# Optimization experiments

Measured on AMD Instinct MI355X. Metric: run time of the kernel, lower is better.

The kernel has to match this reference:

```python
import jax, jax.numpy as jnp
import numpy as np

B, CH, T, D = 16, 64, 2048, 1  # d must be 1 (tf.squeeze(x, axis=-1))
F = 8  # conv filters


def setup_inputs() -> dict:
    key = jax.random.key(0)
    k1, k2, k3, k4 = jax.random.split(key, 4)
    return {
        "x": jax.random.normal(k1, (B, CH, T, D), dtype=jnp.float32),
        "w1": jax.random.normal(k2, (D, F), dtype=jnp.float32) * 0.1,
        "b1": jnp.zeros((F,), dtype=jnp.float32),
        "w2": jax.random.normal(k3, (D, F), dtype=jnp.float32) * 0.1,
        "b2": jnp.zeros((F,), dtype=jnp.float32),
        "gamma": jax.random.normal(k4, (1,), dtype=jnp.float32) * 0.1,
    }


def reference(x, w1, b1, w2, b2, gamma):
    b, ch, t, d = x.shape
    # 1x1 Conv2D == per-position matmul over channel dim; then Permute((2,1,3)) + Reshape((t,-1))
    q = (jnp.matmul(x, w1) + b1)  # (b, ch, t, F)
    k = (jnp.matmul(x, w2) + b2)  # (b, ch, t, F)
    q = jnp.transpose(q, (0, 2, 1, 3)).reshape(b, t, ch * q.shape[-1])  # (b, t, ch*F)
    k = jnp.transpose(k, (0, 2, 1, 3)).reshape(b, t, ch * k.shape[-1])  # (b, t, ch*F)
    energy = jnp.einsum('btf,bsf->bts', q, k)  # (b, t, t)
    max_h = jnp.max(energy, axis=2, keepdims=True)
    min_h = jnp.min(energy, axis=2, keepdims=True)
    energy = (energy - min_h) / (max_h - min_h + 1e-8)
    attention = jax.nn.softmax(energy, axis=-1)  # (b, t, t)
    x_sq = x[..., 0]  # (b, ch, t)
    # matmul(x_sq, attention, transpose_b=True): out[b,c,i] = sum_j x_sq[b,c,j] * attention[b,i,j]
    mixed = jnp.einsum('bcj,bij->bci', x_sq, attention)  # (b, ch, t)
    return gamma[0] * mixed[..., None] + x  # (b, ch, t, 1)
```

## Files before the change

kernel.cpp:

```cpp
#include <hip/hip_runtime.h>

#define NB 16
#define NCH 64
#define NT 2048
#define TI 32
#define TJ 64
#define STR 72

typedef __attribute__((ext_vector_type(8))) short bf8;
typedef __attribute__((ext_vector_type(4))) short bf4;
typedef __attribute__((ext_vector_type(4))) float f4;

static __device__ __forceinline__ short f2b(float f) {
    unsigned u = __float_as_uint(f);
    u += 0x7fffu + ((u >> 16) & 1u);
    return (short)(u >> 16);
}

__global__ __launch_bounds__(256)
void prep_k(const float* __restrict__ x, float* __restrict__ Xs,
            short* __restrict__ xT, short* __restrict__ xn) {
    __shared__ float T[NCH][65];
    const int b = blockIdx.y, t0 = blockIdx.x * 64;
    const int tid = threadIdx.x;
    const float* xb = x + (size_t)b * NCH * NT;

    const int tt = (tid & 15) * 4;
    #pragma unroll
    for (int co = 0; co < 4; ++co) {
        int c = co * 16 + (tid >> 4);
        float4 v = *reinterpret_cast<const float4*>(&xb[(size_t)c * NT + t0 + tt]);
        T[c][tt] = v.x; T[c][tt + 1] = v.y; T[c][tt + 2] = v.z; T[c][tt + 3] = v.w;
        bf4 w; w[0] = f2b(v.x); w[1] = f2b(v.y); w[2] = f2b(v.z); w[3] = f2b(v.w);
        *reinterpret_cast<bf4*>(&xn[((size_t)b * NCH + c) * NT + t0 + tt]) = w;
    }
    __syncthreads();
    if (tid < 64) {
        float s = 0.f;
        #pragma unroll
        for (int c = 0; c < NCH; ++c) s += T[c][tid];
        Xs[b * NT + t0 + tid] = s;
    }
    const int row = tid >> 2, cs = (tid & 3) * 16;
    bf8 v0, v1;
    #pragma unroll
    for (int u = 0; u < 8; ++u) v0[u] = f2b(T[cs + u][row]);
    #pragma unroll
    for (int u = 0; u < 8; ++u) v1[u] = f2b(T[cs + 8 + u][row]);
    short* dst = xT + ((size_t)b * NT + t0 + row) * NCH + cs;
    *reinterpret_cast<bf8*>(dst) = v0;
    *reinterpret_cast<bf8*>(dst + 8) = v1;
}

__global__ __launch_bounds__(256)
void attn3_k(const float* __restrict__ x,
             const float* __restrict__ w1, const float* __restrict__ b1p,
             const float* __restrict__ w2, const float* __restrict__ b2p,
             const float* __restrict__ gp,
             const float* __restrict__ Xs, const short* __restrict__ xT,
             const short* __restrict__ xn,
             float* __restrict__ out) {
    __shared__ short xiT[TI][STR];
    __shared__ short xjT[TJ][STR];
    __shared__ short xjn[NCH][STR];
    __shared__ short P[TI][STR];
    __shared__ float XjL[TJ];
    __shared__ float redA[4][TI], redB[4][TI];
    __shared__ float rowMinL[TI], rowMaxL[TI], rowSumL[TI];

    const int b  = blockIdx.y;
    const int i0 = blockIdx.x * TI;
    const int tid  = threadIdx.x;
    const int wid  = tid >> 6;
    const int lane = tid & 63;
    const int lq   = lane >> 4;
    const int ln   = lane & 15;

    float s11 = 0.f, s1b2 = 0.f, s2b1 = 0.f, sbb = 0.f;
    #pragma unroll
    for (int f = 0; f < 8; ++f) {
        s11  += w1[f] * w2[f];
        s1b2 += w1[f] * b2p[f];
        s2b1 += b1p[f] * w2[f];
        sbb  += b1p[f] * b2p[f];
    }
    const float c0 = (float)NCH * sbb;
    const float g  = gp[0];

    const short* xTb = xT + (size_t)b * NT * NCH;
    const short* xnb = xn + (size_t)b * NCH * NT;
    const float* xb  = x + (size_t)b * NCH * NT;

    {
        const int row = tid >> 3, cs = (tid & 7) * 8;
        *reinterpret_cast<bf8*>(&xiT[row][cs]) =
            *reinterpret_cast<const bf8*>(xTb + (size_t)(i0 + row) * NCH + cs);
    }

    float XiV[2][4];
    #pragma unroll
    for (int mb = 0; mb < 2; ++mb)
        #pragma unroll
        for (int r = 0; r < 4; ++r)
            XiV[mb][r] = Xs[b * NT + i0 + mb * 16 + lq * 4 + r];

    float rmin[2][4], rmax[2][4];
    #pragma unroll
    for (int mb = 0; mb < 2; ++mb)
        #pragma unroll
        for (int r = 0; r < 4; ++r) { rmin[mb][r] = 3.0e38f; rmax[mb][r] = -3.0e38f; }

    for (int j0 = 0; j0 < NT; j0 += TJ) {
        __syncthreads();
        {
            const int row = tid >> 2, cs = (tid & 3) * 16;
            const bf8* src = reinterpret_cast<const bf8*>(xTb + (size_t)(j0 + row) * NCH + cs);
            bf8* dst = reinterpret_cast<bf8*>(&xjT[row][cs]);
            dst[0] = src[0];
            dst[1] = src[1];
        }
        if (tid < 16)
            reinterpret_cast<float4*>(XjL)[tid] =
                reinterpret_cast<const float4*>(Xs + b * NT + j0)[tid];
        __syncthreads();

        bf8 b0 = *reinterpret_cast<const bf8*>(&xjT[wid * 16 + ln][lq * 8]);
        bf8 b1 = *reinterpret_cast<const bf8*>(&xjT[wid * 16 + ln][32 + lq * 8]);
        const float xjv = XjL[wid * 16 + ln];
        #pragma unroll
        for (int mb = 0; mb < 2; ++mb) {
            bf8 a0 = *reinterpret_cast<const bf8*>(&xiT[mb * 16 + ln][lq * 8]);
            bf8 a1 = *reinterpret_cast<const bf8*>(&xiT[mb * 16 + ln][32 + lq * 8]);
            f4 gacc = {0.f, 0.f, 0.f, 0.f};
            gacc = __builtin_amdgcn_mfma_f32_16x16x32_bf16(a0, b0, gacc, 0, 0, 0);
            gacc = __builtin_amdgcn_mfma_f32_16x16x32_bf16(a1, b1, gacc, 0, 0, 0);
            #pragma unroll
            for (int r = 0; r < 4; ++r) {
                float e = fmaf(s11, gacc[r], fmaf(s1b2, XiV[mb][r], fmaf(s2b1, xjv, c0)));
                rmin[mb][r] = fminf(rmin[mb][r], e);
                rmax[mb][r] = fmaxf(rmax[mb][r], e);
            }
        }
    }

    #pragma unroll
    for (int d = 1; d < 16; d <<= 1)
        #pragma unroll
        for (int mb = 0; mb < 2; ++mb)
            #pragma unroll
            for (int r = 0; r < 4; ++r) {
                rmin[mb][r] = fminf(rmin[mb][r], __shfl_xor(rmin[mb][r], d, 64));
                rmax[mb][r] = fmaxf(rmax[mb][r], __shfl_xor(rmax[mb][r], d, 64));
            }
    if (ln == 0)
        #pragma unroll
        for (int mb = 0; mb < 2; ++mb)
            #pragma unroll
            for (int r = 0; r < 4; ++r) {
                redA[wid][mb * 16 + lq * 4 + r] = rmin[mb][r];
                redB[wid][mb * 16 + lq * 4 + r] = rmax[mb][r];
            }
    __syncthreads();
    if (tid < TI) {
        float a = redA[0][tid], bb = redB[0][tid];
        #pragma unroll
        for (int w = 1; w < 4; ++w) {
            a  = fminf(a, redA[w][tid]);
            bb = fmaxf(bb, redB[w][tid]);
        }
        rowMinL[tid] = a;
        rowMaxL[tid] = bb;
    }
    __syncthreads();

    float mn[2][4], inv[2][4];
    #pragma unroll
    for (int mb = 0; mb < 2; ++mb)
        #pragma unroll
        for (int r = 0; r < 4; ++r) {
            const int i = mb * 16 + lq * 4 + r;
            mn[mb][r]  = rowMinL[i];
            inv[mb][r] = 1.f / (rowMaxL[i] - rowMinL[i] + 1e-8f);
        }

    f4 macc[2];
    macc[0] = (f4){0.f, 0.f, 0.f, 0.f};
    macc[1] = (f4){0.f, 0.f, 0.f, 0.f};
    float ps[2][4] = {};

    for (int j0 = 0; j0 < NT; j0 += TJ) {
        __syncthreads();
        {
            const int row = tid >> 2, cs = (tid & 3) * 16;
            const bf8* src = reinterpret_cast<const bf8*>(xTb + (size_t)(j0 + row) * NCH + cs);
            bf8* dst = reinterpret_cast<bf8*>(&xjT[row][cs]);
            dst[0] = src[0];
            dst[1] = src[1];
            const bf8* src2 = reinterpret_cast<const bf8*>(xnb + (size_t)row * NT + j0 + (tid & 3) * 16);
            bf8* dst2 = reinterpret_cast<bf8*>(&xjn[row][(tid & 3) * 16]);
            dst2[0] = src2[0];
            dst2[1] = src2[1];
        }
        if (tid < 16)
            reinterpret_cast<float4*>(XjL)[tid] =
                reinterpret_cast<const float4*>(Xs + b * NT + j0)[tid];
        __syncthreads();

        bf8 b0 = *reinterpret_cast<const bf8*>(&xjT[wid * 16 + ln][lq * 8]);
        bf8 b1 = *reinterpret_cast<const bf8*>(&xjT[wid * 16 + ln][32 + lq * 8]);
        const float xjv = XjL[wid * 16 + ln];
        #pragma unroll
        for (int mb = 0; mb < 2; ++mb) {
            bf8 a0 = *reinterpret_cast<const bf8*>(&xiT[mb * 16 + ln][lq * 8]);
            bf8 a1 = *reinterpret_cast<const bf8*>(&xiT[mb * 16 + ln][32 + lq * 8]);
            f4 gacc = {0.f, 0.f, 0.f, 0.f};
            gacc = __builtin_amdgcn_mfma_f32_16x16x32_bf16(a0, b0, gacc, 0, 0, 0);
            gacc = __builtin_amdgcn_mfma_f32_16x16x32_bf16(a1, b1, gacc, 0, 0, 0);
            #pragma unroll
            for (int r = 0; r < 4; ++r) {
                float e = fmaf(s11, gacc[r], fmaf(s1b2, XiV[mb][r], fmaf(s2b1, xjv, c0)));
                float p = __expf((e - mn[mb][r]) * inv[mb][r]);
                ps[mb][r] += p;
                P[mb * 16 + lq * 4 + r][wid * 16 + ln] = f2b(p);
            }
        }
        __syncthreads();

        bf8 ma0 = *reinterpret_cast<const bf8*>(&xjn[wid * 16 + ln][lq * 8]);
        bf8 ma1 = *reinterpret_cast<const bf8*>(&xjn[wid * 16 + ln][32 + lq * 8]);
        #pragma unroll
        for (int nb = 0; nb < 2; ++nb) {
            bf8 pb0 = *reinterpret_cast<const bf8*>(&P[nb * 16 + ln][lq * 8]);
            bf8 pb1 = *reinterpret_cast<const bf8*>(&P[nb * 16 + ln][32 + lq * 8]);
            macc[nb] = __builtin_amdgcn_mfma_f32_16x16x32_bf16(ma0, pb0, macc[nb], 0, 0, 0);
            macc[nb] = __builtin_amdgcn_mfma_f32_16x16x32_bf16(ma1, pb1, macc[nb], 0, 0, 0);
        }
    }

    #pragma unroll
    for (int d = 1; d < 16; d <<= 1)
        #pragma unroll
        for (int mb = 0; mb < 2; ++mb)
            #pragma unroll
            for (int r = 0; r < 4; ++r)
                ps[mb][r] += __shfl_xor(ps[mb][r], d, 64);
    if (ln == 0)
        #pragma unroll
        for (int mb = 0; mb < 2; ++mb)
            #pragma unroll
            for (int r = 0; r < 4; ++r)
                redA[wid][mb * 16 + lq * 4 + r] = ps[mb][r];
    __syncthreads();
    if (tid < TI) {
        float s = 0.f;
        #pragma unroll
        for (int w = 0; w < 4; ++w) s += redA[w][tid];
        rowSumL[tid] = s;
    }
    __syncthreads();

    #pragma unroll
    for (int nb = 0; nb < 2; ++nb) {
        const int i = i0 + nb * 16 + ln;
        const float rs = rowSumL[nb * 16 + ln];
        #pragma unroll
        for (int r = 0; r < 4; ++r) {
            const int c = wid * 16 + lq * 4 + r;
            const size_t off = ((size_t)b * NCH + c) * NT + i;
            out[off] = g * macc[nb][r] / rs + xb[(size_t)c * NT + i];
        }
    }
}

extern "C" void kernel_launch(void* const* d_in, const int* in_sizes, int n_in,
                              void* d_out, int out_size, void* d_ws, size_t ws_size,
                              hipStream_t stream) {
    const float* x     = (const float*)d_in[0];
    const float* w1    = (const float*)d_in[1];
    const float* b1    = (const float*)d_in[2];
    const float* w2    = (const float*)d_in[3];
    const float* b2    = (const float*)d_in[4];
    const float* gamma = (const float*)d_in[5];
    float* out = (float*)d_out;

    float* Xs = (float*)d_ws;
    short* xT = (short*)((char*)d_ws + (size_t)NB * NT * 4);
    short* xn = (short*)((char*)d_ws + (size_t)NB * NT * 4
                         + (size_t)NB * NT * NCH * 2);

    hipLaunchKernelGGL(prep_k, dim3(NT / 64, NB), dim3(256), 0, stream, x, Xs, xT, xn);
    hipLaunchKernelGGL(attn3_k, dim3(NT / TI, NB), dim3(256), 0, stream,
                       x, w1, b1, w2, b2, gamma, Xs, xT, xn, out);
}
```

Before: 100.3 us.

## Split key dimension across waves and drop per-tile block barriers

Each of the four waves now owns a quarter of the j range and handles all 32 query rows itself. Key and value operands are read straight from global memory into registers, with no cooperative shared-memory staging, and each wave writes its probability tile to a private LDS slice. This removes the two-to-three __syncthreads per j-tile and the shared staging copies. In exchange it adds a cross-wave merge of min/max, row sums and the 64x32 partial accumulators through LDS at the end, plus more global loads per wave and more accumulator registers.

```diff
diff --git a/kernel.cpp b/kernel.cpp
--- a/kernel.cpp
+++ b/kernel.cpp
@@ -3,9 +3,10 @@
 #define NB 16
 #define NCH 64
 #define NT 2048
-#define TI 32
-#define TJ 64
-#define STR 72
+#define SPLIT 4
+#define JQ (NT / SPLIT)
+#define NTILE (JQ / 64)
+#define PSTR 72
 
 typedef __attribute__((ext_vector_type(8))) short bf8;
 typedef __attribute__((ext_vector_type(4))) short bf4;
@@ -53,28 +54,27 @@
 }
 
 __global__ __launch_bounds__(256)
-void attn3_k(const float* __restrict__ x,
+void attn4_k(const float* __restrict__ x,
              const float* __restrict__ w1, const float* __restrict__ b1p,
              const float* __restrict__ w2, const float* __restrict__ b2p,
              const float* __restrict__ gp,
              const float* __restrict__ Xs, const short* __restrict__ xT,
              const short* __restrict__ xn,
              float* __restrict__ out) {
-    __shared__ short xiT[TI][STR];
-    __shared__ short xjT[TJ][STR];
-    __shared__ short xjn[NCH][STR];
-    __shared__ short P[TI][STR];
-    __shared__ float XjL[TJ];
-    __shared__ float redA[4][TI], redB[4][TI];
-    __shared__ float rowMinL[TI], rowMaxL[TI], rowSumL[TI];
+    __shared__ float pool[8192];
+    __shared__ float mergeMn[4][2][16];
+    __shared__ float mergeMx[4][2][16];
+    __shared__ float mergePS[4][2][16];
 
     const int b  = blockIdx.y;
-    const int i0 = blockIdx.x * TI;
+    const int i0 = blockIdx.x * 32;
     const int tid  = threadIdx.x;
-    const int wid  = tid >> 6;
+    const int h    = tid >> 6;
     const int lane = tid & 63;
-    const int lq   = lane >> 4;
-    const int ln   = lane & 15;
+    const int lq = lane >> 4, ln = lane & 15;
+
+    short* Pw = reinterpret_cast<short*>(pool) + h * 32 * PSTR;
+    float* mergeAcc = pool;
 
     float s11 = 0.f, s1b2 = 0.f, s2b1 = 0.f, sbb = 0.f;
     #pragma unroll
@@ -91,183 +91,175 @@
     const short* xnb = xn + (size_t)b * NCH * NT;
     const float* xb  = x + (size_t)b * NCH * NT;
 
-    {
-        const int row = tid >> 3, cs = (tid & 7) * 8;
-        *reinterpret_cast<bf8*>(&xiT[row][cs]) =
-            *reinterpret_cast<const bf8*>(xTb + (size_t)(i0 + row) * NCH + cs);
-    }
-
-    float XiV[2][4];
-    #pragma unroll
-    for (int mb = 0; mb < 2; ++mb)
-        #pragma unroll
-        for (int r = 0; r < 4; ++r)
-            XiV[mb][r] = Xs[b * NT + i0 + mb * 16 + lq * 4 + r];
-
-    float rmin[2][4], rmax[2][4];
-    #pragma unroll
-    for (int mb = 0; mb < 2; ++mb)
-        #pragma unroll
-        for (int r = 0; r < 4; ++r) { rmin[mb][r] = 3.0e38f; rmax[mb][r] = -3.0e38f; }
-
-    for (int j0 = 0; j0 < NT; j0 += TJ) {
-        __syncthreads();
-        {
-            const int row = tid >> 2, cs = (tid & 3) * 16;
-            const bf8* src = reinterpret_cast<const bf8*>(xTb + (size_t)(j0 + row) * NCH + cs);
-            bf8* dst = reinterpret_cast<bf8*>(&xjT[row][cs]);
-            dst[0] = src[0];
-            dst[1] = src[1];
-        }
-        if (tid < 16)
-            reinterpret_cast<float4*>(XjL)[tid] =
-                reinterpret_cast<const float4*>(Xs + b * NT + j0)[tid];
-        __syncthreads();
-
-        bf8 b0 = *reinterpret_cast<const bf8*>(&xjT[wid * 16 + ln][lq * 8]);
-        bf8 b1 = *reinterpret_cast<const bf8*>(&xjT[wid * 16 + ln][32 + lq * 8]);
-        const float xjv = XjL[wid * 16 + ln];
-        #pragma unroll
-        for (int mb = 0; mb < 2; ++mb) {
-            bf8 a0 = *reinterpret_cast<const bf8*>(&xiT[mb * 16 + ln][lq * 8]);
-            bf8 a1 = *reinterpret_cast<const bf8*>(&xiT[mb * 16 + ln][32 + lq * 8]);
-            f4 gacc = {0.f, 0.f, 0.f, 0.f};
-            gacc = __builtin_amdgcn_mfma_f32_16x16x32_bf16(a0, b0, gacc, 0, 0, 0);
-            gacc = __builtin_amdgcn_mfma_f32_16x16x32_bf16(a1, b1, gacc, 0, 0, 0);
-            #pragma unroll
-            for (int r = 0; r < 4; ++r) {
-                float e = fmaf(s11, gacc[r], fmaf(s1b2, XiV[mb][r], fmaf(s2b1, xjv, c0)));
-                rmin[mb][r] = fminf(rmin[mb][r], e);
-                rmax[mb][r] = fmaxf(rmax[mb][r], e);
+    bf8 Bg[2][2];
+    #pragma unroll
+    for (int s = 0; s < 2; ++s)
+        #pragma unroll
+        for (int kk = 0; kk < 2; ++kk)
+            Bg[s][kk] = *reinterpret_cast<const bf8*>(
+                xTb + (size_t)(i0 + s * 16 + ln) * NCH + kk * 32 + lq * 8);
+
+    float cs0[2];
+    #pragma unroll
+    for (int s = 0; s < 2; ++s)
+        cs0[s] = fmaf(s1b2, Xs[b * NT + i0 + s * 16 + ln], c0);
+
+    float rmin[2] = {3.0e38f, 3.0e38f}, rmax[2] = {-3.0e38f, -3.0e38f};
+
+    for (int t = 0; t < NTILE; ++t) {
+        const int j0t = h * JQ + t * 64;
+        const short* abase = xTb + (size_t)j0t * NCH;
+        float XjA[4][4];
+        #pragma unroll
+        for (int jn = 0; jn < 4; ++jn) {
+            float4 v = *reinterpret_cast<const float4*>(Xs + b * NT + j0t + jn * 16 + lq * 4);
+            XjA[jn][0] = v.x; XjA[jn][1] = v.y; XjA[jn][2] = v.z; XjA[jn][3] = v.w;
+        }
+        #pragma unroll
+        for (int jn = 0; jn < 4; ++jn) {
+            const short* ap = abase + (size_t)(jn * 16 + ln) * NCH + lq * 8;
+            bf8 a0 = *reinterpret_cast<const bf8*>(ap);
+            bf8 a1 = *reinterpret_cast<const bf8*>(ap + 32);
+            #pragma unroll
+            for (int s = 0; s < 2; ++s) {
+                f4 acc = {0.f, 0.f, 0.f, 0.f};
+                acc = __builtin_amdgcn_mfma_f32_16x16x32_bf16(a0, Bg[s][0], acc, 0, 0, 0);
+                acc = __builtin_amdgcn_mfma_f32_16x16x32_bf16(a1, Bg[s][1], acc, 0, 0, 0);
+                #pragma unroll
+                for (int r = 0; r < 4; ++r) {
+                    float e = fmaf(s11, acc[r], fmaf(s2b1, XjA[jn][r], cs0[s]));
+                    rmin[s] = fminf(rmin[s], e);
+                    rmax[s] = fmaxf(rmax[s], e);
+                }
             }
         }
     }
 
     #pragma unroll
-    for (int d = 1; d < 16; d <<= 1)
-        #pragma unroll
-        for (int mb = 0; mb < 2; ++mb)
-            #pragma unroll
-            for (int r = 0; r < 4; ++r) {
-                rmin[mb][r] = fminf(rmin[mb][r], __shfl_xor(rmin[mb][r], d, 64));
-                rmax[mb][r] = fmaxf(rmax[mb][r], __shfl_xor(rmax[mb][r], d, 64));
+    for (int s = 0; s < 2; ++s) {
+        rmin[s] = fminf(rmin[s], __shfl_xor(rmin[s], 16, 64));
+        rmin[s] = fminf(rmin[s], __shfl_xor(rmin[s], 32, 64));
+        rmax[s] = fmaxf(rmax[s], __shfl_xor(rmax[s], 16, 64));
+        rmax[s] = fmaxf(rmax[s], __shfl_xor(rmax[s], 32, 64));
+    }
+    if (lane < 16) {
+        #pragma unroll
+        for (int s = 0; s < 2; ++s) {
+            mergeMn[h][s][ln] = rmin[s];
+            mergeMx[h][s][ln] = rmax[s];
+        }
+    }
+    __syncthreads();
+    float mn[2], inv[2];
+    #pragma unroll
+    for (int s = 0; s < 2; ++s) {
+        float a = mergeMn[0][s][ln], bb = mergeMx[0][s][ln];
+        #pragma unroll
+        for (int w = 1; w < 4; ++w) {
+            a  = fminf(a, mergeMn[w][s][ln]);
+            bb = fmaxf(bb, mergeMx[w][s][ln]);
+        }
+        mn[s]  = a;
+        inv[s] = 1.f / (bb - a + 1e-8f);
+    }
+
+    f4 macc[4][2];
+    #pragma unroll
+    for (int cb = 0; cb < 4; ++cb)
+        #pragma unroll
+        for (int s = 0; s < 2; ++s)
+            macc[cb][s] = (f4){0.f, 0.f, 0.f, 0.f};
+    float ps[2] = {0.f, 0.f};
+
+    for (int t = 0; t < NTILE; ++t) {
+        const int j0t = h * JQ + t * 64;
+        const short* abase = xTb + (size_t)j0t * NCH;
+        float XjA[4][4];
+        #pragma unroll
+        for (int jn = 0; jn < 4; ++jn) {
+            float4 v = *reinterpret_cast<const float4*>(Xs + b * NT + j0t + jn * 16 + lq * 4);
+            XjA[jn][0] = v.x; XjA[jn][1] = v.y; XjA[jn][2] = v.z; XjA[jn][3] = v.w;
+        }
+        #pragma unroll
+        for (int jn = 0; jn < 4; ++jn) {
+            const short* ap = abase + (size_t)(jn * 16 + ln) * NCH + lq * 8;
+            bf8 a0 = *reinterpret_cast<const bf8*>(ap);
+            bf8 a1 = *reinterpret_cast<const bf8*>(ap + 32);
+            #pragma unroll
+            for (int s = 0; s < 2; ++s) {
+                f4 acc = {0.f, 0.f, 0.f, 0.f};
+                acc = __builtin_amdgcn_mfma_f32_16x16x32_bf16(a0, Bg[s][0], acc, 0, 0, 0);
+                acc = __builtin_amdgcn_mfma_f32_16x16x32_bf16(a1, Bg[s][1], acc, 0, 0, 0);
+                float p[4];
+                #pragma unroll
+                for (int r = 0; r < 4; ++r) {
+                    float e = fmaf(s11, acc[r], fmaf(s2b1, XjA[jn][r], cs0[s]));
+                    p[r] = __expf((e - mn[s]) * inv[s]);
+                    ps[s] += p[r];
+                }
+                bf4 wv; wv[0] = f2b(p[0]); wv[1] = f2b(p[1]); wv[2] = f2b(p[2]); wv[3] = f2b(p[3]);
+                *reinterpret_cast<bf4*>(&Pw[(s * 16 + ln) * PSTR + jn * 16 + lq * 4]) = wv;
             }
-    if (ln == 0)
-        #pragma unroll
-        for (int mb = 0; mb < 2; ++mb)
-            #pragma unroll
-            for (int r = 0; r < 4; ++r) {
-                redA[wid][mb * 16 + lq * 4 + r] = rmin[mb][r];
-                redB[wid][mb * 16 + lq * 4 + r] = rmax[mb][r];
+        }
+        bf8 Pf[2][2];
+        #pragma unroll
+        for (int s = 0; s < 2; ++s)
+            #pragma unroll
+            for (int kk = 0; kk < 2; ++kk)
+                Pf[s][kk] = *reinterpret_cast<const bf8*>(
+                    &Pw[(s * 16 + ln) * PSTR + kk * 32 + lq * 8]);
+        #pragma unroll
+        for (int cb = 0; cb < 4; ++cb) {
+            const short* mp = xnb + (size_t)(cb * 16 + ln) * NT + j0t + lq * 8;
+            bf8 m0 = *reinterpret_cast<const bf8*>(mp);
+            bf8 m1 = *reinterpret_cast<const bf8*>(mp + 32);
+            #pragma unroll
+            for (int s = 0; s < 2; ++s) {
+                macc[cb][s] = __builtin_amdgcn_mfma_f32_16x16x32_bf16(m0, Pf[s][0], macc[cb][s], 0, 0, 0);
+                macc[cb][s] = __builtin_amdgcn_mfma_f32_16x16x32_bf16(m1, Pf[s][1], macc[cb][s], 0, 0, 0);
             }
-    __syncthreads();
-    if (tid < TI) {
-        float a = redA[0][tid], bb = redB[0][tid];
-        #pragma unroll
-        for (int w = 1; w < 4; ++w) {
-            a  = fminf(a, redA[w][tid]);
-            bb = fmaxf(bb, redB[w][tid]);
-        }
-        rowMinL[tid] = a;
-        rowMaxL[tid] = bb;
-    }
-    __syncthreads();
-
-    float mn[2][4], inv[2][4];
-    #pragma unroll
-    for (int mb = 0; mb < 2; ++mb)
+        }
+    }
+
+    #pragma unroll
+    for (int s = 0; s < 2; ++s) {
+        ps[s] += __shfl_xor(ps[s], 16, 64);
+        ps[s] += __shfl_xor(ps[s], 32, 64);
+    }
+    if (lane < 16) {
+        #pragma unroll
+        for (int s = 0; s < 2; ++s) mergePS[h][s][ln] = ps[s];
+    }
+    __syncthreads();
+    #pragma unroll
+    for (int cb = 0; cb < 4; ++cb)
+        #pragma unroll
+        for (int s = 0; s < 2; ++s)
+            #pragma unroll
+            for (int r = 0; r < 4; ++r)
+                mergeAcc[((size_t)h * 64 + cb * 16 + lq * 4 + r) * 32 + s * 16 + ln] = macc[cb][s][r];
+    __syncthreads();
+
+    float rowSum[2];
+    #pragma unroll
+    for (int s = 0; s < 2; ++s) {
+        float v = 0.f;
+        #pragma unroll
+        for (int w = 0; w < 4; ++w) v += mergePS[w][s][ln];
+        rowSum[s] = v;
+    }
+
+    #pragma unroll
+    for (int s = 0; s < 2; ++s) {
+        const int i = i0 + s * 16 + ln;
         #pragma unroll
         for (int r = 0; r < 4; ++r) {
-            const int i = mb * 16 + lq * 4 + r;
-            mn[mb][r]  = rowMinL[i];
-            inv[mb][r] = 1.f / (rowMaxL[i] - rowMinL[i] + 1e-8f);
-        }
-
-    f4 macc[2];
-    macc[0] = (f4){0.f, 0.f, 0.f, 0.f};
-    macc[1] = (f4){0.f, 0.f, 0.f, 0.f};
-    float ps[2][4] = {};
-
-    for (int j0 = 0; j0 < NT; j0 += TJ) {
-        __syncthreads();
-        {
-            const int row = tid >> 2, cs = (tid & 3) * 16;
-            const bf8* src = reinterpret_cast<const bf8*>(xTb + (size_t)(j0 + row) * NCH + cs);
-            bf8* dst = reinterpret_cast<bf8*>(&xjT[row][cs]);
-            dst[0] = src[0];
-            dst[1] = src[1];
-            const bf8* src2 = reinterpret_cast<const bf8*>(xnb + (size_t)row * NT + j0 + (tid & 3) * 16);
-            bf8* dst2 = reinterpret_cast<bf8*>(&xjn[row][(tid & 3) * 16]);
-            dst2[0] = src2[0];
-            dst2[1] = src2[1];
-        }
-        if (tid < 16)
-            reinterpret_cast<float4*>(XjL)[tid] =
-                reinterpret_cast<const float4*>(Xs + b * NT + j0)[tid];
-        __syncthreads();
-
-        bf8 b0 = *reinterpret_cast<const bf8*>(&xjT[wid * 16 + ln][lq * 8]);
-        bf8 b1 = *reinterpret_cast<const bf8*>(&xjT[wid * 16 + ln][32 + lq * 8]);
-        const float xjv = XjL[wid * 16 + ln];
-        #pragma unroll
-        for (int mb = 0; mb < 2; ++mb) {
-            bf8 a0 = *reinterpret_cast<const bf8*>(&xiT[mb * 16 + ln][lq * 8]);
-            bf8 a1 = *reinterpret_cast<const bf8*>(&xiT[mb * 16 + ln][32 + lq * 8]);
-            f4 gacc = {0.f, 0.f, 0.f, 0.f};
-            gacc = __builtin_amdgcn_mfma_f32_16x16x32_bf16(a0, b0, gacc, 0, 0, 0);
-            gacc = __builtin_amdgcn_mfma_f32_16x16x32_bf16(a1, b1, gacc, 0, 0, 0);
-            #pragma unroll
-            for (int r = 0; r < 4; ++r) {
-                float e = fmaf(s11, gacc[r], fmaf(s1b2, XiV[mb][r], fmaf(s2b1, xjv, c0)));
-                float p = __expf((e - mn[mb][r]) * inv[mb][r]);
-                ps[mb][r] += p;
-                P[mb * 16 + lq * 4 + r][wid * 16 + ln] = f2b(p);
-            }
-        }
-        __syncthreads();
-
-        bf8 ma0 = *reinterpret_cast<const bf8*>(&xjn[wid * 16 + ln][lq * 8]);
-        bf8 ma1 = *reinterpret_cast<const bf8*>(&xjn[wid * 16 + ln][32 + lq * 8]);
-        #pragma unroll
-        for (int nb = 0; nb < 2; ++nb) {
-            bf8 pb0 = *reinterpret_cast<const bf8*>(&P[nb * 16 + ln][lq * 8]);
-            bf8 pb1 = *reinterpret_cast<const bf8*>(&P[nb * 16 + ln][32 + lq * 8]);
-            macc[nb] = __builtin_amdgcn_mfma_f32_16x16x32_bf16(ma0, pb0, macc[nb], 0, 0, 0);
-            macc[nb] = __builtin_amdgcn_mfma_f32_16x16x32_bf16(ma1, pb1, macc[nb], 0, 0, 0);
-        }
-    }
-
-    #pragma unroll
-    for (int d = 1; d < 16; d <<= 1)
-        #pragma unroll
-        for (int mb = 0; mb < 2; ++mb)
-            #pragma unroll
-            for (int r = 0; r < 4; ++r)
-                ps[mb][r] += __shfl_xor(ps[mb][r], d, 64);
-    if (ln == 0)
-        #pragma unroll
-        for (int mb = 0; mb < 2; ++mb)
-            #pragma unroll
-            for (int r = 0; r < 4; ++r)
-                redA[wid][mb * 16 + lq * 4 + r] = ps[mb][r];
-    __syncthreads();
-    if (tid < TI) {
-        float s = 0.f;
-        #pragma unroll
-        for (int w = 0; w < 4; ++w) s += redA[w][tid];
-        rowSumL[tid] = s;
-    }
-    __syncthreads();
-
-    #pragma unroll
-    for (int nb = 0; nb < 2; ++nb) {
-        const int i = i0 + nb * 16 + ln;
-        const float rs = rowSumL[nb * 16 + ln];
-        #pragma unroll
-        for (int r = 0; r < 4; ++r) {
-            const int c = wid * 16 + lq * 4 + r;
-            const size_t off = ((size_t)b * NCH + c) * NT + i;
-            out[off] = g * macc[nb][r] / rs + xb[(size_t)c * NT + i];
+            const int c = h * 16 + lq * 4 + r;
+            float tot = 0.f;
+            #pragma unroll
+            for (int w = 0; w < 4; ++w)
+                tot += mergeAcc[((size_t)w * 64 + c) * 32 + s * 16 + ln];
+            out[((size_t)b * NCH + c) * NT + i] = g * tot / rowSum[s] + xb[(size_t)c * NT + i];
         }
     }
 }
@@ -289,6 +281,6 @@
                          + (size_t)NB * NT * NCH * 2);
 
     hipLaunchKernelGGL(prep_k, dim3(NT / 64, NB), dim3(256), 0, stream, x, Xs, xT, xn);
-    hipLaunchKernelGGL(attn3_k, dim3(NT / TI, NB), dim3(256), 0, stream,
+    hipLaunchKernelGGL(attn4_k, dim3(NT / 32, NB), dim3(256), 0, stream,
                        x, w1, b1, w2, b2, gamma, Xs, xT, xn, out);
 }
```

Result: slower. 107.9 us (+7.5%).
